# Kernel tuning notes

Measured on AMD Instinct MI355X. Metric: run time of the kernel, lower is better.

Reference implementation:

```python
import jax, jax.numpy as jnp
import numpy as np

B, S, HID = 2, 2048, 4096
NH, NKV, HD = 32, 8, 128
MAX_POS = 4096
SCALE = HD ** -0.5


def _rope_tables():
    inv_freq = 1.0 / (10000.0 ** (np.arange(0, HD, 2, dtype=np.float32) / HD))
    t = np.arange(MAX_POS, dtype=np.float32)
    freqs = np.outer(t, inv_freq)              # [MAX_POS, HD/2]
    emb = np.concatenate([freqs, freqs], axis=-1)  # [MAX_POS, HD]
    return jnp.asarray(np.cos(emb)), jnp.asarray(np.sin(emb))


def setup_inputs() -> dict:
    key = jax.random.key(0)
    ks = jax.random.split(key, 6)
    hidden_states = jax.random.normal(ks[0], (B, S, HID), dtype=jnp.float32)
    position_ids = jnp.broadcast_to(jnp.arange(S, dtype=jnp.int64 if jax.config.jax_enable_x64 else jnp.int32), (B, S))
    cos_table, sin_table = _rope_tables()
    # weights stored [in, out] for x @ W
    sd = HID ** -0.5
    Wq = jax.random.normal(ks[1], (HID, NH * HD), dtype=jnp.float32) * sd
    Wk = jax.random.normal(ks[2], (HID, NKV * HD), dtype=jnp.float32) * sd
    Wv = jax.random.normal(ks[3], (HID, NKV * HD), dtype=jnp.float32) * sd
    Wo = jax.random.normal(ks[4], (NH * HD, HID), dtype=jnp.float32) * sd
    return {"hidden_states": hidden_states, "position_ids": position_ids,
            "cos_table": cos_table, "sin_table": sin_table,
            "Wq": Wq, "Wk": Wk, "Wv": Wv, "Wo": Wo}


def _rotate_half(x):
    x1, x2 = jnp.split(x, 2, axis=-1)
    return jnp.concatenate([-x2, x1], axis=-1)


def reference(hidden_states, position_ids, cos_table, sin_table, Wq, Wk, Wv, Wo):
    b, s, _ = hidden_states.shape
    q = (hidden_states @ Wq).reshape(b, s, NH, HD)
    k = (hidden_states @ Wk).reshape(b, s, NKV, HD)
    v = (hidden_states @ Wv).reshape(b, s, NKV, HD)

    # RoPE, cos/sin gathered by position and unsqueezed at head dim (dim=2, bsnd)
    cos = cos_table[position_ids][:, :, None, :]  # [b, s, 1, hd]
    sin = sin_table[position_ids][:, :, None, :]
    q = q * cos + _rotate_half(q) * sin
    k = k * cos + _rotate_half(k) * sin

    # GQA: expand kv heads to match query heads
    rep = NH // NKV
    k = jnp.repeat(k, rep, axis=2)  # [b, s, NH, hd]
    v = jnp.repeat(v, rep, axis=2)

    scores = jnp.einsum('bqnd,bknd->bnqk', q, k) * SCALE  # [b, NH, s, s]
    causal = jnp.tril(jnp.ones((s, s), dtype=bool))
    scores = jnp.where(causal, scores, jnp.finfo(scores.dtype).min)
    probs = jax.nn.softmax(scores, axis=-1)
    attn = jnp.einsum('bnqk,bknd->bqnd', probs, v)  # [b, s, NH, hd]
    attn = attn.reshape(b, s, NH * HD)
    return attn @ Wo
```

## Files before the change

kernel.cpp:

```cpp
#include <hip/hip_runtime.h>
#include <stdint.h>

typedef unsigned short u16;
typedef __bf16 bf16x8 __attribute__((ext_vector_type(8)));
typedef unsigned short u16x8 __attribute__((ext_vector_type(8)));
typedef unsigned short u16x4 __attribute__((ext_vector_type(4)));
typedef float f32x4 __attribute__((ext_vector_type(4)));

#define B_ 2
#define S_ 2048
#define HID_ 4096
#define NH_ 32
#define NKV_ 8
#define HD_ 128
#define NTOT_ 6144
#define SCALE_ 0.08838834764831845f

#define GLD16(gp, lp)                                                     \
  __builtin_amdgcn_global_load_lds(                                       \
      (__attribute__((address_space(1))) void*)(gp),                      \
      (__attribute__((address_space(3))) void*)(lp), 16, 0, 0)

#define BAR __builtin_amdgcn_s_barrier()
#define PRIO1 __builtin_amdgcn_s_setprio(1)
#define PRIO0 __builtin_amdgcn_s_setprio(0)
#define VM8 asm volatile("s_waitcnt vmcnt(8)" ::: "memory")
#define VM0 asm volatile("s_waitcnt vmcnt(0)" ::: "memory")

__device__ __forceinline__ u16 f2b(float f) {
  union { float f; uint32_t u; } v; v.f = f;
  uint32_t u = v.u;
  u = u + 0x7fffu + ((u >> 16) & 1u);
  return (u16)(u >> 16);
}
__device__ __forceinline__ float b2f(u16 s) {
  union { uint32_t u; float f; } v; v.u = ((uint32_t)s) << 16;
  return v.f;
}
__device__ __forceinline__ bf16x8 ldb8(const u16* p) {
  u16x8 u = *(const u16x8*)p;
  return __builtin_bit_cast(bf16x8, u);
}
__device__ __forceinline__ bf16x8 ldb8b(const char* p) {
  u16x8 u = *(const u16x8*)p;
  return __builtin_bit_cast(bf16x8, u);
}

__global__ __launch_bounds__(256) void k_convx(const float* __restrict__ src,
                                               u16* __restrict__ dst, int n4) {
  int i = blockIdx.x * 256 + threadIdx.x;
  if (i >= n4) return;
  const float4 v = ((const float4*)src)[i];
  u16x4 o = { f2b(v.x), f2b(v.y), f2b(v.z), f2b(v.w) };
  *(u16x4*)(dst + (size_t)i * 4) = o;
}

__global__ __launch_bounds__(256) void k_convT(const float* __restrict__ src,
                                               u16* __restrict__ dst, int N, int Kd) {
  __shared__ u16 tile[64][65];
  int k0 = blockIdx.x * 64, n0 = blockIdx.y * 64;
  int t = threadIdx.x;
  int rr = t >> 4;
  int cc = (t & 15) * 4;
#pragma unroll
  for (int p = 0; p < 4; ++p) {
    int r = p * 16 + rr;
    float4 v = *(const float4*)&src[(size_t)(k0 + r) * N + n0 + cc];
    tile[cc + 0][r] = f2b(v.x);
    tile[cc + 1][r] = f2b(v.y);
    tile[cc + 2][r] = f2b(v.z);
    tile[cc + 3][r] = f2b(v.w);
  }
  __syncthreads();
#pragma unroll
  for (int p = 0; p < 4; ++p) {
    int n = p * 16 + rr;
    u16x4 o = { tile[n][cc], tile[n][cc + 1], tile[n][cc + 2], tile[n][cc + 3] };
    *(u16x4*)&dst[(size_t)(n0 + n) * Kd + k0 + cc] = o;
  }
}

__global__ __launch_bounds__(512) void k_gemm_out(const u16* __restrict__ A,
                                                  const u16* __restrict__ Bt,
                                                  float* __restrict__ Cf,
                                                  int M, int N, int Kd) {
  __shared__ __align__(16) char smem[131072];
  const int NT = Kd >> 6;

  int nwg = gridDim.x * gridDim.y;
  int orig = blockIdx.y * gridDim.x + blockIdx.x;
  int cpx = nwg >> 3;
  int swz = (orig & 7) * cpx + (orig >> 3);
  int bx = swz % gridDim.x, by = swz / gridDim.x;
  int m0 = by * 256, n0 = bx * 256;

  int t = threadIdx.x, lane = t & 63, wave = t >> 6;
  int wr = wave >> 2, wc = wave & 3;
  int lg = lane >> 4, l16 = lane & 15;
  int loff = l16 * 64 + ((lg ^ ((l16 >> 1) & 3)) << 4);
  int srow = lane >> 2, schk = (lane & 3) ^ ((lane >> 3) & 3);

  const u16* Asrc = A  + (size_t)(m0 + wave * 32 + srow) * Kd + schk * 8;
  const u16* Bsrc = Bt + (size_t)(n0 + wave * 32 + srow) * Kd + schk * 8;

  f32x4 acc[8][4] = {};

#define OST_A(tile, kc, BB) do {                                              \
    char* d_ = smem + (BB) + ((kc) << 14) + (wave << 11);                     \
    const u16* s_ = Asrc + (size_t)(tile) * 64 + (kc) * 32;                   \
    GLD16(s_, d_); GLD16(s_ + (size_t)16 * Kd, d_ + 1024); } while (0)
#define OST_B(tile, kc, BB) do {                                              \
    char* d_ = smem + (BB) + 32768 + ((kc) << 14) + (wave << 11);             \
    const u16* s_ = Bsrc + (size_t)(tile) * 64 + (kc) * 32;                   \
    GLD16(s_, d_); GLD16(s_ + (size_t)16 * Kd, d_ + 1024); } while (0)
#define OLDB(BB, kc) do { _Pragma("unroll")                                   \
    for (int j = 0; j < 4; ++j)                                               \
      bfr[j] = ldb8b(smem + (BB) + 32768 + ((kc) << 14) + ((wc * 4 + j) << 10) + loff); } while (0)
#define OLDA(BB, kc, mh) do { _Pragma("unroll")                               \
    for (int i = 0; i < 4; ++i)                                               \
      af[i] = ldb8b(smem + (BB) + ((kc) << 14) + ((wr * 8 + (mh) * 4 + i) << 10) + loff); } while (0)
#define OMFMA(mh) do { _Pragma("unroll")                                      \
    for (int i = 0; i < 4; ++i) { _Pragma("unroll")                           \
      for (int j = 0; j < 4; ++j)                                             \
        acc[(mh) * 4 + i][j] = __builtin_amdgcn_mfma_f32_16x16x32_bf16(af[i], bfr[j], acc[(mh) * 4 + i][j], 0, 0, 0); } } while (0)

  OST_A(0, 0, 0); OST_B(0, 0, 0); OST_A(0, 1, 0); OST_B(0, 1, 0);
  OST_A(1, 0, 65536); OST_B(1, 0, 65536);
  VM8; BAR;

  for (int it = 0; it < (NT >> 1); ++it) {
    int a = it << 1;
    bool pf = (a + 2 < NT);
    bf16x8 bfr[4], af[4];
    OLDB(0, 0); OLDA(0, 0, 0); OST_A(a + 1, 1, 65536);
    BAR; PRIO1; OMFMA(0); PRIO0; BAR;
    OLDA(0, 0, 1); OST_B(a + 1, 1, 65536);
    BAR; PRIO1; OMFMA(1); PRIO0; if (pf) { VM8; } else { VM0; } BAR;
    OLDB(0, 1); OLDA(0, 1, 0); if (pf) OST_A(a + 2, 0, 0);
    BAR; PRIO1; OMFMA(0); PRIO0; BAR;
    OLDA(0, 1, 1); if (pf) OST_B(a + 2, 0, 0);
    BAR; PRIO1; OMFMA(1); PRIO0; if (pf) { VM8; } else { VM0; } BAR;
    OLDB(65536, 0); OLDA(65536, 0, 0); if (pf) OST_A(a + 2, 1, 0);
    BAR; PRIO1; OMFMA(0); PRIO0; BAR;
    OLDA(65536, 0, 1); if (pf) OST_B(a + 2, 1, 0);
    BAR; PRIO1; OMFMA(1); PRIO0; if (pf) { VM8; } else { VM0; } BAR;
    OLDB(65536, 1); OLDA(65536, 1, 0); if (pf) OST_A(a + 3, 0, 65536);
    BAR; PRIO1; OMFMA(0); PRIO0; BAR;
    OLDA(65536, 1, 1); if (pf) OST_B(a + 3, 0, 65536);
    BAR; PRIO1; OMFMA(1); PRIO0; if (pf) { VM8; } else { VM0; } BAR;
  }
#undef OST_A
#undef OST_B
#undef OLDB
#undef OLDA
#undef OMFMA

#pragma unroll
  for (int i = 0; i < 8; ++i)
#pragma unroll
    for (int j = 0; j < 4; ++j)
#pragma unroll
      for (int r = 0; r < 4; ++r) {
        int m = m0 + wr * 128 + i * 16 + lg * 4 + r;
        int n = n0 + wc * 64 + j * 16 + l16;
        Cf[(size_t)m * N + n] = acc[i][j][r];
      }
}

__global__ __launch_bounds__(512) void k_gqkv(const u16* __restrict__ A,
                                              const u16* __restrict__ Bt,
                                              u16* __restrict__ Qb,
                                              u16* __restrict__ Kb,
                                              u16* __restrict__ Vb) {
  __shared__ __align__(16) char smem[114688];
  const int Kd = HID_;
  const int NT = Kd >> 6;

  int orig = blockIdx.y * 32 + blockIdx.x;
  int swz = (orig & 7) * 64 + (orig >> 3);
  int bx = swz & 31, by = swz >> 5;
  int m0 = by * 256, n0 = bx * 192;

  int t = threadIdx.x, lane = t & 63, wave = t >> 6;
  int wr = wave >> 2, wc = wave & 3;
  int lg = lane >> 4, l16 = lane & 15;
  int loff = l16 * 64 + ((lg ^ ((l16 >> 1) & 3)) << 4);
  int srow = lane >> 2, schk = (lane & 3) ^ ((lane >> 3) & 3);

  const u16* Asrc = A + (size_t)(m0 + wave * 32 + srow) * Kd + schk * 8;
  const u16* sB0 = Bt + (size_t)(n0 + wave * 16 + srow) * Kd + schk * 8;
  const u16* sB1 = Bt + (size_t)(n0 + 128 + (wave & 3) * 16 + srow) * Kd + schk * 8;
  int bdst2 = (8 + (wave & 3)) << 10;

  f32x4 acc[8][3] = {};

#define QST_A(tile, kc, BB) do {                                              \
    char* d_ = smem + (BB) + ((kc) << 14) + (wave << 11);                     \
    const u16* s_ = Asrc + (size_t)(tile) * 64 + (kc) * 32;                   \
    GLD16(s_, d_); GLD16(s_ + (size_t)16 * Kd, d_ + 1024); } while (0)
#define QST_B(tile, kc, BB) do {                                              \
    char* db_ = smem + (BB) + 32768 + (kc) * 12288;                           \
    GLD16(sB0 + (size_t)(tile) * 64 + (kc) * 32, db_ + (wave << 10));         \
    GLD16(sB1 + (size_t)(tile) * 64 + (kc) * 32, db_ + bdst2); } while (0)
#define QLDB(BB, kc) do { _Pragma("unroll")                                   \
    for (int j = 0; j < 3; ++j)                                               \
      bfr[j] = ldb8b(smem + (BB) + 32768 + (kc) * 12288 + ((wc * 3 + j) << 10) + loff); } while (0)
#define QLDA(BB, kc, mh) do { _Pragma("unroll")                               \
    for (int i = 0; i < 4; ++i)                                               \
      af[i] = ldb8b(smem + (BB) + ((kc) << 14) + ((wr * 8 + (mh) * 4 + i) << 10) + loff); } while (0)
#define QMFMA(mh) do { _Pragma("unroll")                                      \
    for (int i = 0; i < 4; ++i) { _Pragma("unroll")                           \
      for (int j = 0; j < 3; ++j)                                             \
        acc[(mh) * 4 + i][j] = __builtin_amdgcn_mfma_f32_16x16x32_bf16(af[i], bfr[j], acc[(mh) * 4 + i][j], 0, 0, 0); } } while (0)

  QST_A(0, 0, 0); QST_B(0, 0, 0); QST_A(0, 1, 0); QST_B(0, 1, 0);
  QST_A(1, 0, 57344); QST_B(1, 0, 57344);
  VM8; BAR;

  for (int it = 0; it < (NT >> 1); ++it) {
    int a = it << 1;
    bool pf = (a + 2 < NT);
    bf16x8 bfr[3], af[4];
    QLDB(0, 0); QLDA(0, 0, 0); QST_A(a + 1, 1, 57344);
    BAR; PRIO1; QMFMA(0); PRIO0; BAR;
    QLDA(0, 0, 1); QST_B(a + 1, 1, 57344);
    BAR; PRIO1; QMFMA(1); PRIO0; if (pf) { VM8; } else { VM0; } BAR;
    QLDB(0, 1); QLDA(0, 1, 0); if (pf) QST_A(a + 2, 0, 0);
    BAR; PRIO1; QMFMA(0); PRIO0; BAR;
    QLDA(0, 1, 1); if (pf) QST_B(a + 2, 0, 0);
    BAR; PRIO1; QMFMA(1); PRIO0; if (pf) { VM8; } else { VM0; } BAR;
    QLDB(57344, 0); QLDA(57344, 0, 0); if (pf) QST_A(a + 2, 1, 0);
    BAR; PRIO1; QMFMA(0); PRIO0; BAR;
    QLDA(57344, 0, 1); if (pf) QST_B(a + 2, 1, 0);
    BAR; PRIO1; QMFMA(1); PRIO0; if (pf) { VM8; } else { VM0; } BAR;
    QLDB(57344, 1); QLDA(57344, 1, 0); if (pf) QST_A(a + 3, 0, 57344);
    BAR; PRIO1; QMFMA(0); PRIO0; BAR;
    QLDA(57344, 1, 1); if (pf) QST_B(a + 3, 0, 57344);
    BAR; PRIO1; QMFMA(1); PRIO0; if (pf) { VM8; } else { VM0; } BAR;
  }
#undef QST_A
#undef QST_B
#undef QLDB
#undef QLDA
#undef QMFMA

#pragma unroll
  for (int i = 0; i < 8; ++i)
#pragma unroll
    for (int j = 0; j < 3; ++j)
#pragma unroll
      for (int r = 0; r < 4; ++r) {
        int m = m0 + wr * 128 + i * 16 + lg * 4 + r;
        int n = n0 + wc * 48 + j * 16 + l16;
        int head = n >> 7, d = n & 127;
        int b = m >> 11, s = m & (S_ - 1);
        u16 val = f2b(acc[i][j][r]);
        if (head < NH_) {
          Qb[(((size_t)b * NH_ + head) * S_ + s) * HD_ + d] = val;
        } else if (head < NH_ + NKV_) {
          Kb[(((size_t)b * NKV_ + (head - NH_)) * S_ + s) * HD_ + d] = val;
        } else {
          Vb[(((size_t)b * NKV_ + (head - NH_ - NKV_)) * HD_ + d) * S_ + s] = val;
        }
      }
}

__global__ __launch_bounds__(256) void k_rope(u16* __restrict__ buf, const int* __restrict__ pos,
                                              const float* __restrict__ ct, const float* __restrict__ st,
                                              int H, int rows) {
  int wave = threadIdx.x >> 6, lane = threadIdx.x & 63;
  int row = blockIdx.x * 4 + wave;
  if (row >= rows) return;
  int s = row & (S_ - 1);
  int b = row / (H * S_);
  int p = pos[b * S_ + s];
  size_t base = (size_t)row * HD_;
  float x1 = b2f(buf[base + lane]);
  float x2 = b2f(buf[base + 64 + lane]);
  float c  = ct[(size_t)p * HD_ + lane];
  float sn = st[(size_t)p * HD_ + lane];
  buf[base + lane]      = f2b(x1 * c - x2 * sn);
  buf[base + 64 + lane] = f2b(x2 * c + x1 * sn);
}

__global__ __launch_bounds__(256, 4) void k_attn(const u16* __restrict__ Q,
                                                 const u16* __restrict__ K,
                                                 const u16* __restrict__ Vt,
                                                 u16* __restrict__ Ob) {
  __shared__ __align__(16) char smem[40960];
  const int VS_OFF = 16384, PS_OFF = 32768;

  int bid = blockIdx.x;
  int pid = bid & 15;
  int h   = (bid >> 4) & 31;
  int b   = bid >> 9;
  int kvh = h >> 2;
  int tid = threadIdx.x;
  int wave = tid >> 6, lane = tid & 63;
  int lg = lane >> 4, l16 = lane & 15;
  int lsw = (l16 & 7) << 4;

  const u16* Qp = Q  + (((size_t)b * NH_  + h)   * S_) * HD_;
  const u16* Kp = K  + (((size_t)b * NKV_ + kvh) * S_) * HD_;
  const u16* Vp = Vt + (((size_t)b * NKV_ + kvh) * HD_) * S_;

  for (int pass = 0; pass < 2; ++pass) {
    int qt = pass ? (31 - pid) : pid;
    int q0 = qt * 64 + wave * 16;
    int qg = q0 + l16;

    bf16x8 qf[4];
#pragma unroll
    for (int c = 0; c < 4; ++c)
      qf[c] = ldb8(&Qp[(size_t)qg * HD_ + c * 32 + lg * 8]);

    f32x4 oacc[8] = {};
    float mrun = -1e30f, lrun = 0.f;

    int nt = qt + 1;
    for (int tI = 0; tI < nt; ++tI) {
      int kb = tI * 64;
      __syncthreads();
#pragma unroll
      for (int i = 0; i < 4; ++i) {
        int ci = i * 256 + tid;
        int r = ci >> 4, ch = ci & 15;
        u16x8 v = *(const u16x8*)&Kp[(size_t)(kb + r) * HD_ + ch * 8];
        *(u16x8*)(smem + r * 256 + ((ch * 16) ^ ((r & 7) << 4))) = v;
      }
#pragma unroll
      for (int i = 0; i < 4; ++i) {
        int ci = i * 256 + tid;
        int r = ci >> 3, ch = ci & 7;
        u16x8 v = *(const u16x8*)&Vp[(size_t)r * S_ + kb + ch * 8];
        *(u16x8*)(smem + VS_OFF + r * 128 + ((ch * 16) ^ ((r & 7) << 4))) = v;
      }
      __syncthreads();

      f32x4 sc[4] = {};
#pragma unroll
      for (int c = 0; c < 4; ++c) {
#pragma unroll
        for (int n = 0; n < 4; ++n) {
          bf16x8 kf = ldb8b(smem + (n * 16 + l16) * 256 + ((c * 64 + lg * 16) ^ lsw));
          sc[n] = __builtin_amdgcn_mfma_f32_16x16x32_bf16(kf, qf[c], sc[n], 0, 0, 0);
        }
      }

      bool diag = (tI == qt);
      float mx = -1e30f;
#pragma unroll
      for (int n = 0; n < 4; ++n)
#pragma unroll
        for (int r = 0; r < 4; ++r) {
          float v = sc[n][r];
          int key = kb + n * 16 + lg * 4 + r;
          if (diag && key > qg) v = -1e30f;
          sc[n][r] = v;
          mx = fmaxf(mx, v);
        }
      mx = fmaxf(mx, __shfl_xor(mx, 16));
      mx = fmaxf(mx, __shfl_xor(mx, 32));
      float mnew = fmaxf(mrun, mx * SCALE_);
      float alpha = __expf(mrun - mnew);
      float ps = 0.f;
#pragma unroll
      for (int n = 0; n < 4; ++n) {
        u16x4 pk;
#pragma unroll
        for (int r = 0; r < 4; ++r) {
          float p = __expf(fmaf(sc[n][r], SCALE_, -mnew));
          ps += p;
          pk[r] = f2b(p);
        }
        *(u16x4*)(smem + PS_OFF + wave * 2048 + l16 * 128 + ((n * 32 + lg * 8) ^ lsw)) = pk;
      }
      ps += __shfl_xor(ps, 16);
      ps += __shfl_xor(ps, 32);
      lrun = lrun * alpha + ps;
      mrun = mnew;

      float ar[4];
#pragma unroll
      for (int r = 0; r < 4; ++r) ar[r] = __shfl(alpha, lg * 4 + r);
#pragma unroll
      for (int ns = 0; ns < 8; ++ns)
#pragma unroll
        for (int r = 0; r < 4; ++r) oacc[ns][r] *= ar[r];

#pragma unroll
      for (int ck = 0; ck < 2; ++ck) {
        bf16x8 pa = ldb8b(smem + PS_OFF + wave * 2048 + l16 * 128 + ((ck * 64 + lg * 16) ^ lsw));
#pragma unroll
        for (int ns = 0; ns < 8; ++ns) {
          bf16x8 vf = ldb8b(smem + VS_OFF + (ns * 16 + l16) * 128 + ((ck * 64 + lg * 16) ^ lsw));
          oacc[ns] = __builtin_amdgcn_mfma_f32_16x16x32_bf16(pa, vf, oacc[ns], 0, 0, 0);
        }
      }
    }

    float lr[4];
#pragma unroll
    for (int r = 0; r < 4; ++r) lr[r] = 1.0f / __shfl(lrun, lg * 4 + r);
#pragma unroll
    for (int ns = 0; ns < 8; ++ns)
#pragma unroll
      for (int r = 0; r < 4; ++r) {
        int q = q0 + lg * 4 + r;
        Ob[((size_t)(b * S_) + q) * (NH_ * HD_) + h * HD_ + ns * 16 + l16] =
            f2b(oacc[ns][r] * lr[r]);
      }
  }
}

extern "C" void kernel_launch(void* const* d_in, const int* in_sizes, int n_in,
                              void* d_out, int out_size, void* d_ws, size_t ws_size,
                              hipStream_t stream) {
  const float* hs  = (const float*)d_in[0];
  const int*   pos = (const int*)d_in[1];
  const float* ct  = (const float*)d_in[2];
  const float* st  = (const float*)d_in[3];
  const float* Wq  = (const float*)d_in[4];
  const float* Wk  = (const float*)d_in[5];
  const float* Wv  = (const float*)d_in[6];
  const float* Wo  = (const float*)d_in[7];
  float* out = (float*)d_out;

  char* w = (char*)d_ws;
  u16* Xb    = (u16*)(w);
  u16* WqkvT = (u16*)(w + 33554432ull);
  u16* WoT   = (u16*)(w + 83886080ull);
  u16* Qb    = (u16*)(w + 117440512ull);
  u16* Kb    = (u16*)(w + 150994944ull);
  u16* Vb    = (u16*)(w + 159383552ull);
  u16* Attb  = (u16*)(w + 167772160ull);

  k_convx<<<16384, 256, 0, stream>>>(hs, Xb, 4194304);
  k_convT<<<dim3(64, 64), 256, 0, stream>>>(Wq, WqkvT, 4096, 4096);
  k_convT<<<dim3(64, 16), 256, 0, stream>>>(Wk, WqkvT + (size_t)4096 * 4096, 1024, 4096);
  k_convT<<<dim3(64, 16), 256, 0, stream>>>(Wv, WqkvT + (size_t)5120 * 4096, 1024, 4096);
  k_convT<<<dim3(64, 64), 256, 0, stream>>>(Wo, WoT, 4096, 4096);
  k_gqkv<<<dim3(32, 16), 512, 0, stream>>>(Xb, WqkvT, Qb, Kb, Vb);
  k_rope<<<32768, 256, 0, stream>>>(Qb, pos, ct, st, NH_, B_ * NH_ * S_);
  k_rope<<<8192, 256, 0, stream>>>(Kb, pos, ct, st, NKV_, B_ * NKV_ * S_);
  k_attn<<<1024, 256, 0, stream>>>(Qb, Kb, Vb, Attb);
  k_gemm_out<<<dim3(16, 16), 512, 0, stream>>>(Attb, WoT, out, 4096, 4096, 4096);
}
```

Before: 616.0 us.

## Restructure GEMM pipeline into single-barrier phases with full A fragment preload

Both bf16 GEMM kernels (output projection and fused QKV) now run each k-chunk as one phase. Each phase loads all A and B fragments from LDS, issues the next chunk's global-to-LDS copies, waits with vmcnt(4), crosses one barrier and runs all MFMAs for that chunk. This halves the barrier count per chunk and shortens the prefetch distance to one chunk ahead instead of the previous deeper staging. It keeps more fragments live in registers, and the shallower prefetch may expose more global latency.

```diff
diff --git a/kernel.cpp b/kernel.cpp
--- a/kernel.cpp
+++ b/kernel.cpp
@@ -24,7 +24,7 @@
 #define BAR __builtin_amdgcn_s_barrier()
 #define PRIO1 __builtin_amdgcn_s_setprio(1)
 #define PRIO0 __builtin_amdgcn_s_setprio(0)
-#define VM8 asm volatile("s_waitcnt vmcnt(8)" ::: "memory")
+#define VM4 asm volatile("s_waitcnt vmcnt(4)" ::: "memory")
 #define VM0 asm volatile("s_waitcnt vmcnt(0)" ::: "memory")
 
 __device__ __forceinline__ u16 f2b(float f) {
@@ -113,47 +113,44 @@
     char* d_ = smem + (BB) + 32768 + ((kc) << 14) + (wave << 11);             \
     const u16* s_ = Bsrc + (size_t)(tile) * 64 + (kc) * 32;                   \
     GLD16(s_, d_); GLD16(s_ + (size_t)16 * Kd, d_ + 1024); } while (0)
-#define OLDB(BB, kc) do { _Pragma("unroll")                                   \
+
+#define OPH(BB, kc, tl, OB, DS) do {                                          \
+    bf16x8 bfr[4], af0[4], af1[4];                                            \
+    _Pragma("unroll")                                                         \
     for (int j = 0; j < 4; ++j)                                               \
-      bfr[j] = ldb8b(smem + (BB) + 32768 + ((kc) << 14) + ((wc * 4 + j) << 10) + loff); } while (0)
-#define OLDA(BB, kc, mh) do { _Pragma("unroll")                               \
+      bfr[j] = ldb8b(smem + (BB) + 32768 + ((kc) << 14) + ((wc * 4 + j) << 10) + loff); \
+    _Pragma("unroll")                                                         \
     for (int i = 0; i < 4; ++i)                                               \
-      af[i] = ldb8b(smem + (BB) + ((kc) << 14) + ((wr * 8 + (mh) * 4 + i) << 10) + loff); } while (0)
-#define OMFMA(mh) do { _Pragma("unroll")                                      \
+      af0[i] = ldb8b(smem + (BB) + ((kc) << 14) + ((wr * 8 + i) << 10) + loff); \
+    _Pragma("unroll")                                                         \
+    for (int i = 0; i < 4; ++i)                                               \
+      af1[i] = ldb8b(smem + (BB) + ((kc) << 14) + ((wr * 8 + 4 + i) << 10) + loff); \
+    if (DS) { OST_A(tl, kc, OB); OST_B(tl, kc, OB); VM4; } else { VM0; }      \
+    BAR; PRIO1;                                                               \
+    _Pragma("unroll")                                                         \
     for (int i = 0; i < 4; ++i) { _Pragma("unroll")                           \
       for (int j = 0; j < 4; ++j)                                             \
-        acc[(mh) * 4 + i][j] = __builtin_amdgcn_mfma_f32_16x16x32_bf16(af[i], bfr[j], acc[(mh) * 4 + i][j], 0, 0, 0); } } while (0)
+        acc[i][j] = __builtin_amdgcn_mfma_f32_16x16x32_bf16(af0[i], bfr[j], acc[i][j], 0, 0, 0); } \
+    _Pragma("unroll")                                                         \
+    for (int i = 0; i < 4; ++i) { _Pragma("unroll")                           \
+      for (int j = 0; j < 4; ++j)                                             \
+        acc[4 + i][j] = __builtin_amdgcn_mfma_f32_16x16x32_bf16(af1[i], bfr[j], acc[4 + i][j], 0, 0, 0); } \
+    PRIO0; } while (0)
 
   OST_A(0, 0, 0); OST_B(0, 0, 0); OST_A(0, 1, 0); OST_B(0, 1, 0);
-  OST_A(1, 0, 65536); OST_B(1, 0, 65536);
-  VM8; BAR;
+  VM4; BAR;
 
   for (int it = 0; it < (NT >> 1); ++it) {
     int a = it << 1;
     bool pf = (a + 2 < NT);
-    bf16x8 bfr[4], af[4];
-    OLDB(0, 0); OLDA(0, 0, 0); OST_A(a + 1, 1, 65536);
-    BAR; PRIO1; OMFMA(0); PRIO0; BAR;
-    OLDA(0, 0, 1); OST_B(a + 1, 1, 65536);
-    BAR; PRIO1; OMFMA(1); PRIO0; if (pf) { VM8; } else { VM0; } BAR;
-    OLDB(0, 1); OLDA(0, 1, 0); if (pf) OST_A(a + 2, 0, 0);
-    BAR; PRIO1; OMFMA(0); PRIO0; BAR;
-    OLDA(0, 1, 1); if (pf) OST_B(a + 2, 0, 0);
-    BAR; PRIO1; OMFMA(1); PRIO0; if (pf) { VM8; } else { VM0; } BAR;
-    OLDB(65536, 0); OLDA(65536, 0, 0); if (pf) OST_A(a + 2, 1, 0);
-    BAR; PRIO1; OMFMA(0); PRIO0; BAR;
-    OLDA(65536, 0, 1); if (pf) OST_B(a + 2, 1, 0);
-    BAR; PRIO1; OMFMA(1); PRIO0; if (pf) { VM8; } else { VM0; } BAR;
-    OLDB(65536, 1); OLDA(65536, 1, 0); if (pf) OST_A(a + 3, 0, 65536);
-    BAR; PRIO1; OMFMA(0); PRIO0; BAR;
-    OLDA(65536, 1, 1); if (pf) OST_B(a + 3, 0, 65536);
-    BAR; PRIO1; OMFMA(1); PRIO0; if (pf) { VM8; } else { VM0; } BAR;
+    OPH(0,     0, a + 1, 65536, true);
+    OPH(0,     1, a + 1, 65536, true);
+    OPH(65536, 0, a + 2, 0,     pf);
+    OPH(65536, 1, a + 2, 0,     pf);
   }
+#undef OPH
 #undef OST_A
 #undef OST_B
-#undef OLDB
-#undef OLDA
-#undef OMFMA
 
 #pragma unroll
   for (int i = 0; i < 8; ++i)
@@ -202,47 +199,44 @@
     char* db_ = smem + (BB) + 32768 + (kc) * 12288;                           \
     GLD16(sB0 + (size_t)(tile) * 64 + (kc) * 32, db_ + (wave << 10));         \
     GLD16(sB1 + (size_t)(tile) * 64 + (kc) * 32, db_ + bdst2); } while (0)
-#define QLDB(BB, kc) do { _Pragma("unroll")                                   \
+
+#define QPH(BB, kc, tl, OB, DS) do {                                          \
+    bf16x8 bfr[3], af0[4], af1[4];                                            \
+    _Pragma("unroll")                                                         \
     for (int j = 0; j < 3; ++j)                                               \
-      bfr[j] = ldb8b(smem + (BB) + 32768 + (kc) * 12288 + ((wc * 3 + j) << 10) + loff); } while (0)
-#define QLDA(BB, kc, mh) do { _Pragma("unroll")                               \
+      bfr[j] = ldb8b(smem + (BB) + 32768 + (kc) * 12288 + ((wc * 3 + j) << 10) + loff); \
+    _Pragma("unroll")                                                         \
     for (int i = 0; i < 4; ++i)                                               \
-      af[i] = ldb8b(smem + (BB) + ((kc) << 14) + ((wr * 8 + (mh) * 4 + i) << 10) + loff); } while (0)
-#define QMFMA(mh) do { _Pragma("unroll")                                      \
+      af0[i] = ldb8b(smem + (BB) + ((kc) << 14) + ((wr * 8 + i) << 10) + loff); \
+    _Pragma("unroll")                                                         \
+    for (int i = 0; i < 4; ++i)                                               \
+      af1[i] = ldb8b(smem + (BB) + ((kc) << 14) + ((wr * 8 + 4 + i) << 10) + loff); \
+    if (DS) { QST_A(tl, kc, OB); QST_B(tl, kc, OB); VM4; } else { VM0; }      \
+    BAR; PRIO1;                                                               \
+    _Pragma("unroll")                                                         \
     for (int i = 0; i < 4; ++i) { _Pragma("unroll")                           \
       for (int j = 0; j < 3; ++j)                                             \
-        acc[(mh) * 4 + i][j] = __builtin_amdgcn_mfma_f32_16x16x32_bf16(af[i], bfr[j], acc[(mh) * 4 + i][j], 0, 0, 0); } } while (0)
+        acc[i][j] = __builtin_amdgcn_mfma_f32_16x16x32_bf16(af0[i], bfr[j], acc[i][j], 0, 0, 0); } \
+    _Pragma("unroll")                                                         \
+    for (int i = 0; i < 4; ++i) { _Pragma("unroll")                           \
+      for (int j = 0; j < 3; ++j)                                             \
+        acc[4 + i][j] = __builtin_amdgcn_mfma_f32_16x16x32_bf16(af1[i], bfr[j], acc[4 + i][j], 0, 0, 0); } \
+    PRIO0; } while (0)
 
   QST_A(0, 0, 0); QST_B(0, 0, 0); QST_A(0, 1, 0); QST_B(0, 1, 0);
-  QST_A(1, 0, 57344); QST_B(1, 0, 57344);
-  VM8; BAR;
+  VM4; BAR;
 
   for (int it = 0; it < (NT >> 1); ++it) {
     int a = it << 1;
     bool pf = (a + 2 < NT);
-    bf16x8 bfr[3], af[4];
-    QLDB(0, 0); QLDA(0, 0, 0); QST_A(a + 1, 1, 57344);
-    BAR; PRIO1; QMFMA(0); PRIO0; BAR;
-    QLDA(0, 0, 1); QST_B(a + 1, 1, 57344);
-    BAR; PRIO1; QMFMA(1); PRIO0; if (pf) { VM8; } else { VM0; } BAR;
-    QLDB(0, 1); QLDA(0, 1, 0); if (pf) QST_A(a + 2, 0, 0);
-    BAR; PRIO1; QMFMA(0); PRIO0; BAR;
-    QLDA(0, 1, 1); if (pf) QST_B(a + 2, 0, 0);
-    BAR; PRIO1; QMFMA(1); PRIO0; if (pf) { VM8; } else { VM0; } BAR;
-    QLDB(57344, 0); QLDA(57344, 0, 0); if (pf) QST_A(a + 2, 1, 0);
-    BAR; PRIO1; QMFMA(0); PRIO0; BAR;
-    QLDA(57344, 0, 1); if (pf) QST_B(a + 2, 1, 0);
-    BAR; PRIO1; QMFMA(1); PRIO0; if (pf) { VM8; } else { VM0; } BAR;
-    QLDB(57344, 1); QLDA(57344, 1, 0); if (pf) QST_A(a + 3, 0, 57344);
-    BAR; PRIO1; QMFMA(0); PRIO0; BAR;
-    QLDA(57344, 1, 1); if (pf) QST_B(a + 3, 0, 57344);
-    BAR; PRIO1; QMFMA(1); PRIO0; if (pf) { VM8; } else { VM0; } BAR;
+    QPH(0,     0, a + 1, 57344, true);
+    QPH(0,     1, a + 1, 57344, true);
+    QPH(57344, 0, a + 2, 0,     pf);
+    QPH(57344, 1, a + 2, 0,     pf);
   }
+#undef QPH
 #undef QST_A
 #undef QST_B
-#undef QLDB
-#undef QLDA
-#undef QMFMA
 
 #pragma unroll
   for (int i = 0; i < 8; ++i)
```

Result: no change. 617.5 us (+0.2%).
